# Kernel tuning notes

Hardware: AMD Instinct MI355X
Metric: run time of the kernel (lower is better)

Reference implementation:

```python
import jax, jax.numpy as jnp
import numpy as np

B, L, H, K = 4, 4096, 2048, 4
EPS = 1e-5

def setup_inputs() -> dict:
    key = jax.random.key(0)
    k1, k2, k3, k4 = jax.random.split(key, 4)
    x = jax.random.normal(k1, (B, L, H), dtype=jnp.float32)
    # depthwise Conv1d weight: (out_channels=H, in_channels/groups=1, K)
    w = jax.random.normal(k2, (H, 1, K), dtype=jnp.float32) * (1.0 / np.sqrt(K))
    gamma = jax.random.uniform(k3, (H,), dtype=jnp.float32, minval=0.5, maxval=1.5)
    beta = jax.random.normal(k4, (H,), dtype=jnp.float32) * 0.05
    return {"x": x, "w": w, "gamma": gamma, "beta": beta}

def reference(x, w, gamma, beta):
    # x: (B, L, H) -> (B, H, L) channels-first like torch Conv1d
    xc = jnp.transpose(x, (0, 2, 1))
    k = w.shape[-1]
    h = w.shape[0]
    # causal depthwise conv: left-pad K-1, groups = H
    y = jax.lax.conv_general_dilated(
        xc, w,
        window_strides=(1,),
        padding=[(k - 1, 0)],
        feature_group_count=h,
        dimension_numbers=("NCH", "OIH", "NCH"),
    )
    # residual: x_padded[:, :, K-1:] == original xc
    y = y + xc
    y = jnp.transpose(y, (0, 2, 1))  # (B, L, H)
    # LayerNorm over hidden dim
    mu = jnp.mean(y, axis=-1, keepdims=True)
    var = jnp.mean(jnp.square(y - mu), axis=-1, keepdims=True)
    out = (y - mu) * jax.lax.rsqrt(var + EPS) * gamma + beta
    return out
```

## Files before the change

kernel.cpp:

```cpp
#include <hip/hip_runtime.h>

constexpr int B = 4;
constexpr int L = 4096;
constexpr int H = 2048;
constexpr int KTAP = 4;
constexpr float EPS = 1e-5f;

constexpr int THREADS = 256;
constexpr int H4 = H / 4;
constexpr int VPT = H4 / THREADS;

__global__ __launch_bounds__(THREADS)
void fused_conv_res_ln(const float* __restrict__ x,
                       const float* __restrict__ w,
                       const float* __restrict__ gamma,
                       const float* __restrict__ beta,
                       float* __restrict__ out)
{
    const int row = blockIdx.x;
    const int b   = row / L;
    const int l   = row - b * L;
    const int t   = threadIdx.x;

    const float4* x4  = reinterpret_cast<const float4*>(x) + (size_t)(b) * L * H4;
    const float4* w4  = reinterpret_cast<const float4*>(w);
    const float4* g4  = reinterpret_cast<const float4*>(gamma);
    const float4* bt4 = reinterpret_cast<const float4*>(beta);
    float4* o4 = reinterpret_cast<float4*>(out) + (size_t)row * H4;

    float y[VPT][4];
    float sum = 0.f, sumsq = 0.f;

    #pragma unroll
    for (int v = 0; v < VPT; ++v) {
        const int j = t + v * THREADS;

        float4 xr[KTAP];
        #pragma unroll
        for (int r = 0; r < KTAP; ++r) {
            const int lr = l - (KTAP - 1) + r;
            if (lr >= 0) {
                xr[r] = x4[(size_t)lr * H4 + j];
            } else {
                xr[r] = make_float4(0.f, 0.f, 0.f, 0.f);
            }
        }

        const float4 wc0 = w4[4 * j + 0];
        const float4 wc1 = w4[4 * j + 1];
        const float4 wc2 = w4[4 * j + 2];
        const float4 wc3 = w4[4 * j + 3];

        float y0 = xr[0].x * wc0.x + xr[1].x * wc0.y + xr[2].x * wc0.z + xr[3].x * wc0.w + xr[3].x;
        float y1 = xr[0].y * wc1.x + xr[1].y * wc1.y + xr[2].y * wc1.z + xr[3].y * wc1.w + xr[3].y;
        float y2 = xr[0].z * wc2.x + xr[1].z * wc2.y + xr[2].z * wc2.z + xr[3].z * wc2.w + xr[3].z;
        float y3 = xr[0].w * wc3.x + xr[1].w * wc3.y + xr[2].w * wc3.z + xr[3].w * wc3.w + xr[3].w;

        y[v][0] = y0; y[v][1] = y1; y[v][2] = y2; y[v][3] = y3;

        sum   += y0 + y1 + y2 + y3;
        sumsq += y0 * y0 + y1 * y1 + y2 * y2 + y3 * y3;
    }

    #pragma unroll
    for (int off = 32; off > 0; off >>= 1) {
        sum   += __shfl_down(sum,   off, 64);
        sumsq += __shfl_down(sumsq, off, 64);
    }
    __shared__ float s_sum[THREADS / 64];
    __shared__ float s_sq [THREADS / 64];
    const int wave = t >> 6;
    const int lane = t & 63;
    if (lane == 0) { s_sum[wave] = sum; s_sq[wave] = sumsq; }
    __syncthreads();

    float tot = 0.f, totsq = 0.f;
    #pragma unroll
    for (int i = 0; i < THREADS / 64; ++i) { tot += s_sum[i]; totsq += s_sq[i]; }

    const float inv_h = 1.0f / (float)H;
    const float mu    = tot * inv_h;
    const float var   = totsq * inv_h - mu * mu;
    const float rstd  = rsqrtf(var + EPS);

    #pragma unroll
    for (int v = 0; v < VPT; ++v) {
        const int j = t + v * THREADS;
        const float4 g = g4[j];
        const float4 be = bt4[j];
        float4 o;
        o.x = (y[v][0] - mu) * rstd * g.x + be.x;
        o.y = (y[v][1] - mu) * rstd * g.y + be.y;
        o.z = (y[v][2] - mu) * rstd * g.z + be.z;
        o.w = (y[v][3] - mu) * rstd * g.w + be.w;
        o4[j] = o;
    }
}

extern "C" void kernel_launch(void* const* d_in, const int* in_sizes, int n_in,
                              void* d_out, int out_size, void* d_ws, size_t ws_size,
                              hipStream_t stream) {
    const float* x     = (const float*)d_in[0];
    const float* w     = (const float*)d_in[1];
    const float* gamma = (const float*)d_in[2];
    const float* beta  = (const float*)d_in[3];
    float* out = (float*)d_out;

    dim3 grid(B * L);
    dim3 block(THREADS);
    fused_conv_res_ln<<<grid, block, 0, stream>>>(x, w, gamma, beta, out);
}
```

Measured before the change: 284.8 us.

## Process 8 rows per block with sliding register window and XCD-aware tile mapping

Result: faster. 249.0 us (-12.6%).

```diff
diff --git a/kernel.cpp b/kernel.cpp
--- a/kernel.cpp
+++ b/kernel.cpp
@@ -8,105 +8,126 @@
 
 constexpr int THREADS = 256;
 constexpr int H4 = H / 4;
-constexpr int VPT = H4 / THREADS;
+constexpr int COLS = H4 / THREADS;
+constexpr int ROWS = 8;
+constexpr int TILES = (B * L) / ROWS;
+constexpr int TPB = L / ROWS;
+constexpr int NXCD = 8;
+constexpr int WAVES = THREADS / 64;
 
 __global__ __launch_bounds__(THREADS)
-void fused_conv_res_ln(const float* __restrict__ x,
-                       const float* __restrict__ w,
-                       const float* __restrict__ gamma,
-                       const float* __restrict__ beta,
-                       float* __restrict__ out)
+void fused_conv_res_ln(const float4* __restrict__ x4,
+                       const float4* __restrict__ w4,
+                       const float4* __restrict__ g4,
+                       const float4* __restrict__ bt4,
+                       float4* __restrict__ o4)
 {
-    const int row = blockIdx.x;
-    const int b   = row / L;
-    const int l   = row - b * L;
-    const int t   = threadIdx.x;
+    const int bid     = blockIdx.x;
+    const int logical = (bid & (NXCD - 1)) * (TILES / NXCD) + (bid >> 3);
+    const int b       = logical / TPB;
+    const int tile    = logical - b * TPB;
+    const int l0      = tile * ROWS;
+    const int t       = threadIdx.x;
 
-    const float4* x4  = reinterpret_cast<const float4*>(x) + (size_t)(b) * L * H4;
-    const float4* w4  = reinterpret_cast<const float4*>(w);
-    const float4* g4  = reinterpret_cast<const float4*>(gamma);
-    const float4* bt4 = reinterpret_cast<const float4*>(beta);
-    float4* o4 = reinterpret_cast<float4*>(out) + (size_t)row * H4;
+    const size_t rowbase = (size_t)b * L;
 
-    float y[VPT][4];
-    float sum = 0.f, sumsq = 0.f;
+    float4 xw[COLS][KTAP];
+    float4 wc[COLS][4];
+    float4 gg[COLS], bb[COLS];
+    int    jj[COLS];
 
     #pragma unroll
-    for (int v = 0; v < VPT; ++v) {
-        const int j = t + v * THREADS;
+    for (int c = 0; c < COLS; ++c) {
+        const int j = t + c * THREADS;
+        jj[c] = j;
+        #pragma unroll
+        for (int k = 0; k < 4; ++k) wc[c][k] = w4[4 * j + k];
+        gg[c] = g4[j];
+        bb[c] = bt4[j];
+        #pragma unroll
+        for (int k = 0; k < 3; ++k) {
+            const int lr = l0 - 3 + k;
+            xw[c][k] = (lr >= 0) ? x4[(rowbase + lr) * H4 + j]
+                                 : make_float4(0.f, 0.f, 0.f, 0.f);
+        }
+        xw[c][3] = x4[(rowbase + l0) * H4 + j];
+    }
 
-        float4 xr[KTAP];
-        #pragma unroll
-        for (int r = 0; r < KTAP; ++r) {
-            const int lr = l - (KTAP - 1) + r;
-            if (lr >= 0) {
-                xr[r] = x4[(size_t)lr * H4 + j];
-            } else {
-                xr[r] = make_float4(0.f, 0.f, 0.f, 0.f);
-            }
+    __shared__ float s_sum[ROWS][WAVES];
+    __shared__ float s_sq [ROWS][WAVES];
+    const int wave = t >> 6;
+    const int lane = t & 63;
+
+    #pragma unroll
+    for (int r = 0; r < ROWS; ++r) {
+        float4 xn[COLS];
+        if (r + 1 < ROWS) {
+            #pragma unroll
+            for (int c = 0; c < COLS; ++c)
+                xn[c] = x4[(rowbase + l0 + r + 1) * H4 + jj[c]];
         }
 
-        const float4 wc0 = w4[4 * j + 0];
-        const float4 wc1 = w4[4 * j + 1];
-        const float4 wc2 = w4[4 * j + 2];
-        const float4 wc3 = w4[4 * j + 3];
+        float y[COLS][4];
+        float sum = 0.f, sq = 0.f;
+        #pragma unroll
+        for (int c = 0; c < COLS; ++c) {
+            const float4 a0 = xw[c][0], a1 = xw[c][1], a2 = xw[c][2], a3 = xw[c][3];
+            y[c][0] = a0.x * wc[c][0].x + a1.x * wc[c][0].y + a2.x * wc[c][0].z + a3.x * wc[c][0].w + a3.x;
+            y[c][1] = a0.y * wc[c][1].x + a1.y * wc[c][1].y + a2.y * wc[c][1].z + a3.y * wc[c][1].w + a3.y;
+            y[c][2] = a0.z * wc[c][2].x + a1.z * wc[c][2].y + a2.z * wc[c][2].z + a3.z * wc[c][2].w + a3.z;
+            y[c][3] = a0.w * wc[c][3].x + a1.w * wc[c][3].y + a2.w * wc[c][3].z + a3.w * wc[c][3].w + a3.w;
+            sum += y[c][0] + y[c][1] + y[c][2] + y[c][3];
+            sq  += y[c][0] * y[c][0] + y[c][1] * y[c][1]
+                 + y[c][2] * y[c][2] + y[c][3] * y[c][3];
+        }
 
-        float y0 = xr[0].x * wc0.x + xr[1].x * wc0.y + xr[2].x * wc0.z + xr[3].x * wc0.w + xr[3].x;
-        float y1 = xr[0].y * wc1.x + xr[1].y * wc1.y + xr[2].y * wc1.z + xr[3].y * wc1.w + xr[3].y;
-        float y2 = xr[0].z * wc2.x + xr[1].z * wc2.y + xr[2].z * wc2.z + xr[3].z * wc2.w + xr[3].z;
-        float y3 = xr[0].w * wc3.x + xr[1].w * wc3.y + xr[2].w * wc3.z + xr[3].w * wc3.w + xr[3].w;
+        #pragma unroll
+        for (int off = 32; off > 0; off >>= 1) {
+            sum += __shfl_down(sum, off, 64);
+            sq  += __shfl_down(sq,  off, 64);
+        }
+        if (lane == 0) { s_sum[r][wave] = sum; s_sq[r][wave] = sq; }
+        __syncthreads();
 
-        y[v][0] = y0; y[v][1] = y1; y[v][2] = y2; y[v][3] = y3;
+        float tot = 0.f, totq = 0.f;
+        #pragma unroll
+        for (int i = 0; i < WAVES; ++i) { tot += s_sum[r][i]; totq += s_sq[r][i]; }
 
-        sum   += y0 + y1 + y2 + y3;
-        sumsq += y0 * y0 + y1 * y1 + y2 * y2 + y3 * y3;
-    }
+        const float inv_h = 1.0f / (float)H;
+        const float mu    = tot * inv_h;
+        const float var   = totq * inv_h - mu * mu;
+        const float rstd  = rsqrtf(var + EPS);
 
-    #pragma unroll
-    for (int off = 32; off > 0; off >>= 1) {
-        sum   += __shfl_down(sum,   off, 64);
-        sumsq += __shfl_down(sumsq, off, 64);
-    }
-    __shared__ float s_sum[THREADS / 64];
-    __shared__ float s_sq [THREADS / 64];
-    const int wave = t >> 6;
-    const int lane = t & 63;
-    if (lane == 0) { s_sum[wave] = sum; s_sq[wave] = sumsq; }
-    __syncthreads();
+        #pragma unroll
+        for (int c = 0; c < COLS; ++c) {
+            float4 o;
+            o.x = (y[c][0] - mu) * rstd * gg[c].x + bb[c].x;
+            o.y = (y[c][1] - mu) * rstd * gg[c].y + bb[c].y;
+            o.z = (y[c][2] - mu) * rstd * gg[c].z + bb[c].z;
+            o.w = (y[c][3] - mu) * rstd * gg[c].w + bb[c].w;
+            o4[(rowbase + l0 + r) * H4 + jj[c]] = o;
+        }
 
-    float tot = 0.f, totsq = 0.f;
-    #pragma unroll
-    for (int i = 0; i < THREADS / 64; ++i) { tot += s_sum[i]; totsq += s_sq[i]; }
-
-    const float inv_h = 1.0f / (float)H;
-    const float mu    = tot * inv_h;
-    const float var   = totsq * inv_h - mu * mu;
-    const float rstd  = rsqrtf(var + EPS);
-
-    #pragma unroll
-    for (int v = 0; v < VPT; ++v) {
-        const int j = t + v * THREADS;
-        const float4 g = g4[j];
-        const float4 be = bt4[j];
-        float4 o;
-        o.x = (y[v][0] - mu) * rstd * g.x + be.x;
-        o.y = (y[v][1] - mu) * rstd * g.y + be.y;
-        o.z = (y[v][2] - mu) * rstd * g.z + be.z;
-        o.w = (y[v][3] - mu) * rstd * g.w + be.w;
-        o4[j] = o;
+        #pragma unroll
+        for (int c = 0; c < COLS; ++c) {
+            xw[c][0] = xw[c][1];
+            xw[c][1] = xw[c][2];
+            xw[c][2] = xw[c][3];
+            if (r + 1 < ROWS) xw[c][3] = xn[c];
+        }
     }
 }
 
 extern "C" void kernel_launch(void* const* d_in, const int* in_sizes, int n_in,
                               void* d_out, int out_size, void* d_ws, size_t ws_size,
                               hipStream_t stream) {
-    const float* x     = (const float*)d_in[0];
-    const float* w     = (const float*)d_in[1];
-    const float* gamma = (const float*)d_in[2];
-    const float* beta  = (const float*)d_in[3];
-    float* out = (float*)d_out;
+    const float4* x     = (const float4*)d_in[0];
+    const float4* w     = (const float4*)d_in[1];
+    const float4* gamma = (const float4*)d_in[2];
+    const float4* beta  = (const float4*)d_in[3];
+    float4* out = (float4*)d_out;
 
-    dim3 grid(B * L);
+    dim3 grid(TILES);
     dim3 block(THREADS);
     fused_conv_res_ln<<<grid, block, 0, stream>>>(x, w, gamma, beta, out);
 }
```
